# Kernel tuning notes

Hardware: AMD Instinct MI355X
Metric: run time of the kernel (lower is better)

The kernel has to match this reference:

```python
import jax, jax.numpy as jnp
import numpy as np

C = 5          # max within-cluster spike gap (module-level constant in source repo)
DELTA = 0.05   # margin constant (module-level constant in source repo)
B, T, N = 128, 512, 256


def setup_inputs() -> dict:
    key = jax.random.key(0)
    k1, k2, k3 = jax.random.split(key, 3)
    vmem = jax.random.normal(k1, (B, T, N), dtype=jnp.float32) - 1.5
    vlastmem = jax.random.normal(k2, (B, T, N), dtype=jnp.float32)  # unused by the loss math
    labels_t = jax.random.randint(k3, (B, N), 0, 4)
    ratio = jnp.float32(0.5)
    return {"vmem": vmem, "vlastmem": vlastmem, "labels_t": labels_t, "ratio": ratio}


def _per_neuron(v, key):
    """v: [T] membrane trace for one (batch, neuron). Returns (num_cluster, under_term, max_over)."""
    Tn = v.shape[0]
    t = jnp.arange(Tn)
    spike = v >= 0.0
    s = spike.astype(jnp.int32)
    # prefix sums: cs[i] = number of spikes in v[:i]
    cs = jnp.concatenate([jnp.zeros(1, jnp.int32), jnp.cumsum(s)])
    # new cluster starts at t iff spike[t] and no spike in [t-C, t-1]  (gap > C)
    prev_cnt = cs[t] - cs[jnp.clip(t - C, 0, Tn)]
    is_start = spike & (prev_cnt == 0)
    nclu = jnp.sum(is_start.astype(jnp.int32))
    # under-branch mask = union over clusters of [first-C, last+C] = C-dilation of spike train
    dil_cnt = cs[jnp.clip(t + C + 1, 0, Tn)] - cs[jnp.clip(t - C, 0, Tn)]
    mask = dil_cnt > 0

    # per-cluster stats via segmented reductions (cluster id = running count of starts)
    cid = jnp.clip(jnp.cumsum(is_start.astype(jnp.int32)) - 1, 0, Tn - 1)
    counts = jax.ops.segment_sum(s, cid, num_segments=Tn)
    first = jax.ops.segment_min(jnp.where(spike, t, Tn), cid, num_segments=Tn)
    last = jax.ops.segment_max(jnp.where(spike, t, -1), cid, num_segments=Tn)

    # over branch: cluster minimizing (end_idx - beg_idx) == min spike count (first on ties)
    counts_q = jnp.where(t < nclu, counts, Tn + 2)
    ic = jnp.argmin(counts_q)
    over_mask = (t >= first[ic]) & (t <= last[ic])
    max_over = jnp.max(jnp.where(over_mask, v, -jnp.inf))

    # under branch: if unmasked timesteps remain, penalize -max(v[mask==0]);
    # else take v at a (pinned-seed) random spike position
    has_zero = jnp.any(~mask)
    max_unmask = jnp.max(jnp.where(~mask, v, -jnp.inf))
    nsp = cs[-1]
    sorted_pos = jnp.sort(jnp.where(spike, t, Tn))
    r = jax.random.randint(key, (), 0, jnp.maximum(nsp, 1))
    v_rand = v[jnp.clip(sorted_pos[r], 0, Tn - 1)]
    under_term = jnp.where(has_zero, -max_unmask, v_rand)
    return nclu, under_term, max_over


def _forward(vmem, vlastmem, labels_t, ratio):
    Bv, Tv, Nv = vmem.shape
    vflat = jnp.swapaxes(vmem, 1, 2).reshape(Bv * Nv, Tv)   # [B*N, T]
    lflat = labels_t.reshape(Bv * Nv)
    keys = jax.random.split(jax.random.key(42), Bv * Nv)     # pinned seed for the random-spike pick
    nclu, under_term, max_over = jax.vmap(_per_neuron)(vflat, keys)
    ncf = nclu.astype(vmem.dtype)
    margin = DELTA * ratio * ncf
    under = jnp.where(lflat > nclu, under_term + margin, 0.0)
    over = jnp.where(lflat < nclu, max_over + margin, 0.0)
    loss = jnp.sum(under + over)
    spike_output = ncf.reshape(Bv, Nv)
    return loss, spike_output


def reference(vmem, vlastmem, labels_t, ratio):
    return _forward(vmem, vlastmem, labels_t, ratio)
```

## Files before the change

### kernel.cpp

```cpp
#include <hip/hip_runtime.h>
#include <stdint.h>

#define TDIM 512
#define NDIM 256
#define CGAP 5
#define DELTA_C 0.05f
#define NSEG 8
#define SEGT 64
#define BIGI (1 << 28)

extern "C" __global__ void __launch_bounds__(512, 2)
stca_kernel(const float* __restrict__ vmem, const int* __restrict__ labels,
            const float* __restrict__ ratio_p, float* __restrict__ out) {
  __shared__ int   si[9][NSEG * 64];
  __shared__ float sf[6][NSEG * 64];

  const int lane = threadIdx.x & 63;
  const int seg  = threadIdx.x >> 6;
  const int blk  = blockIdx.x;
  const int b    = blk >> 2;
  const int n0   = (blk & 3) << 6;
  const int n    = n0 + lane;

  const float* g = vmem + (size_t)b * TDIM * NDIM + n;
  const int t0 = seg * SEGT, t1 = t0 + SEGT;

  int   last_spike = -1000, nclu = 0, cur_cnt = 0, cur_fs = 0, fs = BIGI;
  float cur_max = -INFINITY, cur_maxlast = -INFINITY;
  float seg_run_max = -INFINITY, mfs_snap = -INFINITY;
  int   pfx_cnt = 0, pfx_ls = 0;
  float pfx_core = -INFINITY, pfx_mfs = -INFINITY;
  int   bint_cnt = BIGI;
  float bint_max = -INFINITY;
  unsigned hist = 0u;
  float umax = -INFINITY;
  int   has_un = 0;
  float vd0 = 0.f, vd1 = 0.f, vd2 = 0.f, vd3 = 0.f, vd4 = 0.f, vd5 = 0.f;

  if (t0 > 0) {
#pragma unroll
    for (int j = 0; j < CGAP; ++j) {
      const float v = g[(size_t)(t0 - CGAP + j) * NDIM];
      hist = ((hist << 1) | (v >= 0.f ? 1u : 0u)) & 0x7FFu;
    }
  }

  auto step = [&](float v, int te) {
    const bool spike   = v >= 0.0f;
    const bool isstart = spike && ((te - last_spike) > CGAP);
    const bool closing = isstart && (nclu > 0);
    const bool isfirst = closing && (nclu == 1);
    const bool bet     = closing && (nclu > 1) && (cur_cnt < bint_cnt);
    pfx_cnt  = isfirst ? cur_cnt     : pfx_cnt;
    pfx_ls   = isfirst ? last_spike  : pfx_ls;
    pfx_core = isfirst ? cur_maxlast : pfx_core;
    pfx_mfs  = isfirst ? mfs_snap    : pfx_mfs;
    bint_cnt = bet ? cur_cnt     : bint_cnt;
    bint_max = bet ? cur_maxlast : bint_max;
    nclu += isstart ? 1 : 0;
    cur_fs  = isstart ? te : cur_fs;
    cur_max = isstart ? v : fmaxf(cur_max, v);
    cur_maxlast = spike ? cur_max : cur_maxlast;
    cur_cnt = (isstart ? 0 : cur_cnt) + (spike ? 1 : 0);
    seg_run_max = fmaxf(seg_run_max, v);
    const bool snap = spike && (nclu == 1);
    mfs_snap = snap ? seg_run_max : mfs_snap;
    fs = (spike && fs == BIGI) ? te : fs;
    last_spike = spike ? te : last_spike;
    hist = ((hist << 1) | (spike ? 1u : 0u)) & 0x7FFu;
    vd5 = vd4; vd4 = vd3; vd3 = vd2; vd2 = vd1; vd1 = vd0; vd0 = v;
    const bool un = (hist == 0u) && (te >= t0 + CGAP);
    umax = un ? fmaxf(umax, vd5) : umax;
    has_un |= un ? 1 : 0;
  };

#pragma unroll 1
  for (int c = 0; c < SEGT / 8; ++c) {
    const float* gp = g + (size_t)(t0 + c * 8) * NDIM;
    const float y0 = gp[0 * NDIM], y1 = gp[1 * NDIM], y2 = gp[2 * NDIM],
                y3 = gp[3 * NDIM], y4 = gp[4 * NDIM], y5 = gp[5 * NDIM],
                y6 = gp[6 * NDIM], y7 = gp[7 * NDIM];
    const int tc = t0 + c * 8;
    step(y0, tc + 0); step(y1, tc + 1); step(y2, tc + 2); step(y3, tc + 3);
    step(y4, tc + 4); step(y5, tc + 5); step(y6, tc + 6); step(y7, tc + 7);
  }

#pragma unroll
  for (int j = 0; j < CGAP; ++j) {
    const int te = t1 + j;
    const float v = (te < TDIM) ? g[(size_t)te * NDIM] : -INFINITY;
    const bool spike = v >= 0.0f;
    hist = ((hist << 1) | (spike ? 1u : 0u)) & 0x7FFu;
    vd5 = vd4; vd4 = vd3; vd3 = vd2; vd2 = vd1; vd1 = vd0; vd0 = v;
    const bool un = (hist == 0u);
    umax = un ? fmaxf(umax, vd5) : umax;
    has_un |= un ? 1 : 0;
  }

  int   sfx_cnt = 0, sfx_fs = 0;
  float sfx_core = -INFINITY, sfx_mte = -INFINITY;
  if (nclu >= 1) {
    sfx_cnt = cur_cnt; sfx_fs = cur_fs; sfx_core = cur_maxlast; sfx_mte = cur_max;
    if (nclu == 1) {
      pfx_cnt = cur_cnt; pfx_ls = last_spike; pfx_core = cur_maxlast; pfx_mfs = mfs_snap;
    }
  }

  const int idx = threadIdx.x;
  si[0][idx] = nclu;   si[1][idx] = fs;      si[2][idx] = last_spike;
  si[3][idx] = pfx_cnt; si[4][idx] = pfx_ls; si[5][idx] = sfx_cnt;
  si[6][idx] = sfx_fs;  si[7][idx] = bint_cnt; si[8][idx] = has_un;
  sf[0][idx] = pfx_core; sf[1][idx] = pfx_mfs; sf[2][idx] = sfx_core;
  sf[3][idx] = sfx_mte;  sf[4][idx] = bint_max; sf[5][idx] = umax;
  __syncthreads();

  if (seg != 0) return;

  int   a_nclu = nclu, a_fs = fs, a_ls = last_spike;
  int   a_pcnt = pfx_cnt, a_pls = pfx_ls, a_scnt = sfx_cnt, a_sfs = sfx_fs;
  int   a_bcnt = bint_cnt, a_hun = has_un;
  float a_pcore = pfx_core, a_pmfs = pfx_mfs, a_score = sfx_core, a_smte = sfx_mte;
  float a_bmax = bint_max, a_umax = umax;

  for (int s = 1; s < NSEG; ++s) {
    const int j = (s << 6) + lane;
    const int   r_nclu = si[0][j], r_fs = si[1][j], r_ls = si[2][j];
    const int   r_pcnt = si[3][j], r_pls = si[4][j];
    const int   r_scnt = si[5][j], r_sfs = si[6][j];
    const int   r_bcnt = si[7][j], r_hun = si[8][j];
    const float r_pcore = sf[0][j], r_pmfs = sf[1][j];
    const float r_score = sf[2][j], r_smte = sf[3][j];
    const float r_bmax = sf[4][j], r_umax = sf[5][j];

    a_umax = fmaxf(a_umax, r_umax);
    a_hun |= r_hun;
    if (r_nclu == 0) continue;
    if (a_nclu == 0) {
      a_nclu = r_nclu; a_fs = r_fs; a_ls = r_ls;
      a_pcnt = r_pcnt; a_pls = r_pls; a_pcore = r_pcore; a_pmfs = r_pmfs;
      a_scnt = r_scnt; a_sfs = r_sfs; a_score = r_score; a_smte = r_smte;
      a_bcnt = r_bcnt; a_bmax = r_bmax;
      continue;
    }
    if (r_fs - a_ls <= CGAP) {
      const int   Bc    = a_scnt + r_pcnt;
      const float Bcore = fmaxf(a_smte, r_pmfs);
      const float Bmfs  = fmaxf(fmaxf(a_pmfs, a_smte), r_pmfs);
      const float Bmte  = fmaxf(fmaxf(a_smte, r_pmfs), r_smte);
      const int   Bfs = a_sfs, Bls = r_pls;
      int nb = a_bcnt; float nbm = a_bmax;
      if (a_nclu >= 2 && r_nclu >= 2 && Bc < nb) { nb = Bc; nbm = Bcore; }
      if (r_bcnt < nb) { nb = r_bcnt; nbm = r_bmax; }
      if (a_nclu == 1) { a_pcnt = Bc; a_pls = Bls; a_pcore = Bcore; a_pmfs = Bmfs; }
      if (r_nclu == 1) { a_scnt = Bc; a_sfs = Bfs; a_score = Bcore; a_smte = Bmte; }
      else             { a_scnt = r_scnt; a_sfs = r_sfs; a_score = r_score; a_smte = r_smte; }
      a_bcnt = nb; a_bmax = nbm;
      a_nclu = a_nclu + r_nclu - 1;
      a_ls = r_ls;
    } else {
      int nb = a_bcnt; float nbm = a_bmax;
      if (a_nclu >= 2 && a_scnt < nb) { nb = a_scnt; nbm = a_score; }
      if (r_nclu >= 2 && r_pcnt < nb) { nb = r_pcnt; nbm = r_pcore; }
      if (r_bcnt < nb) { nb = r_bcnt; nbm = r_bmax; }
      a_bcnt = nb; a_bmax = nbm;
      a_scnt = r_scnt; a_sfs = r_sfs; a_score = r_score; a_smte = r_smte;
      a_nclu += r_nclu;
      a_ls = r_ls;
    }
  }

  int bc = a_pcnt; float bm = a_pcore;
  if (a_nclu >= 2) {
    if (a_bcnt < bc) { bc = a_bcnt; bm = a_bmax; }
    if (a_scnt < bc) { bc = a_scnt; bm = a_score; }
  }

  const float ratio = ratio_p[0];
  const int   label = labels[b * NDIM + n];
  const float ncf    = (float)a_nclu;
  const float margin = DELTA_C * ratio * ncf;
  const float under_term = a_hun ? (-a_umax) : 0.0f;
  const float under = (label > a_nclu) ? (under_term + margin) : 0.0f;
  const float over  = (label < a_nclu) ? (bm + margin) : 0.0f;

  out[1 + b * NDIM + n] = ncf;

  float sum = under + over;
#pragma unroll
  for (int off = 32; off > 0; off >>= 1) sum += __shfl_down(sum, off);
  if (lane == 0) atomicAdd(out, sum);
}

extern "C" void kernel_launch(void* const* d_in, const int* in_sizes, int n_in,
                              void* d_out, int out_size, void* d_ws,
                              size_t ws_size, hipStream_t stream) {
  const float* vmem   = (const float*)d_in[0];
  const int*   labels = (const int*)d_in[2];
  const float* ratio  = (const float*)d_in[3];
  float* out = (float*)d_out;

  hipMemsetAsync(d_out, 0, sizeof(float), stream);
  dim3 grid(512);
  dim3 block(512);
  hipLaunchKernelGGL(stca_kernel, grid, block, 0, stream, vmem, labels, ratio,
                     out);
}
```

Measured before the change: 147.7 us.

## Split scan into bitmask-based segment kernel plus finalize kernel

Replaces the sequential per-timestep state machine with a two-kernel scheme. Each thread loads 32 timesteps, builds a spike bitmask, and uses popcount, ctz/clz and bit dilation to get cluster starts, counts and masked maxima. Partial summaries are merged within the block, written to workspace across four time quarters, and combined by a second finalize kernel that also computes the loss with a block-level reduction before the atomic add. This raises parallelism over time and removes the serial dependency chain, at the cost of an extra launch and a workspace round trip.

```diff
diff --git a/kernel.cpp b/kernel.cpp
--- a/kernel.cpp
+++ b/kernel.cpp
@@ -5,190 +5,254 @@
 #define NDIM 256
 #define CGAP 5
 #define DELTA_C 0.05f
-#define NSEG 8
-#define SEGT 64
 #define BIGI (1 << 28)
 
+typedef unsigned long long u64;
+typedef unsigned int u32;
+
+
+__device__ __forceinline__ int ctz32(u32 x) { return x ? __builtin_ctz(x) : 32; }
+__device__ __forceinline__ int hib32(u32 x) { return x ? 31 - __builtin_clz(x) : -1; }
+__device__ __forceinline__ u32 below32(int p) { return (p >= 32) ? ~0u : ((1u << p) - 1u); }
+__device__ __forceinline__ u32 rmask(int lo, int hi) { return below32(hi + 1) & ~below32(lo); }
+
+struct Sum {
+  int nclu, fs, ls, pcnt, pls, scnt, sfs, bcnt;
+  float pcore, pmfs, score, smte, bmax, umax;
+};
+
+__device__ __forceinline__ void sum_init(Sum& a) {
+  a.nclu = 0; a.fs = BIGI; a.ls = 0; a.pcnt = 0; a.pls = 0; a.scnt = 0;
+  a.sfs = 0; a.bcnt = BIGI;
+  a.pcore = -INFINITY; a.pmfs = -INFINITY; a.score = -INFINITY;
+  a.smte = -INFINITY; a.bmax = -INFINITY; a.umax = -INFINITY;
+}
+
+__device__ __forceinline__ void merge(Sum& a, const Sum& r) {
+  a.umax = fmaxf(a.umax, r.umax);
+  if (r.nclu == 0) return;
+  if (a.nclu == 0) { const float um = a.umax; a = r; a.umax = um; return; }
+  if (r.fs - a.ls <= CGAP) {
+    const int   Bc    = a.scnt + r.pcnt;
+    const float Bcore = fmaxf(a.smte, r.pmfs);
+    const float Bmfs  = fmaxf(fmaxf(a.pmfs, a.smte), r.pmfs);
+    const float Bmte  = fmaxf(fmaxf(a.smte, r.pmfs), r.smte);
+    const int   Bfs = a.sfs, Bls = r.pls;
+    int nb = a.bcnt; float nbm = a.bmax;
+    if (a.nclu >= 2 && r.nclu >= 2 && Bc < nb) { nb = Bc; nbm = Bcore; }
+    if (r.bcnt < nb) { nb = r.bcnt; nbm = r.bmax; }
+    if (a.nclu == 1) { a.pcnt = Bc; a.pls = Bls; a.pcore = Bcore; a.pmfs = Bmfs; }
+    if (r.nclu == 1) { a.scnt = Bc; a.sfs = Bfs; a.score = Bcore; a.smte = Bmte; }
+    else             { a.scnt = r.scnt; a.sfs = r.sfs; a.score = r.score; a.smte = r.smte; }
+    a.bcnt = nb; a.bmax = nbm;
+    a.nclu += r.nclu - 1;
+    a.ls = r.ls;
+  } else {
+    int nb = a.bcnt; float nbm = a.bmax;
+    if (a.nclu >= 2 && a.scnt < nb) { nb = a.scnt; nbm = a.score; }
+    if (r.nclu >= 2 && r.pcnt < nb) { nb = r.pcnt; nbm = r.pcore; }
+    if (r.bcnt < nb) { nb = r.bcnt; nbm = r.bmax; }
+    a.bcnt = nb; a.bmax = nbm;
+    a.scnt = r.scnt; a.sfs = r.sfs; a.score = r.score; a.smte = r.smte;
+    a.nclu += r.nclu;
+    a.ls = r.ls;
+  }
+}
+
+extern "C" __global__ void __launch_bounds__(256, 8)
+stca_seg(const float* __restrict__ vmem, float* __restrict__ ws) {
+  __shared__ u32 shS[256];
+  __shared__ u32 shA0[256], shA1[256];
+  __shared__ float shF[6][256];
+
+  const int tid = threadIdx.x, lane = tid & 63, w = tid >> 6;
+  const int blk = blockIdx.x;
+  const int tq = blk & 3, nq = (blk >> 2) & 3, b = blk >> 4;
+  const int n = (nq << 6) + lane;
+  const int t0 = (tq << 7) + (w << 5);
+  const float* g = vmem + (size_t)b * TDIM * NDIM + n;
+  const float* gp = g + (size_t)t0 * NDIM;
+
+#define LD(i) const float v##i = gp[(i) * NDIM];
+  LD(0)  LD(1)  LD(2)  LD(3)  LD(4)  LD(5)  LD(6)  LD(7)
+  LD(8)  LD(9)  LD(10) LD(11) LD(12) LD(13) LD(14) LD(15)
+  LD(16) LD(17) LD(18) LD(19) LD(20) LD(21) LD(22) LD(23)
+  LD(24) LD(25) LD(26) LD(27) LD(28) LD(29) LD(30) LD(31)
+#undef LD
+
+  u32 left5 = 0, right5 = 0;
+  if (w == 0 && tq > 0) {
+#pragma unroll
+    for (int j = 0; j < CGAP; ++j)
+      left5 |= (g[(size_t)(t0 - CGAP + j) * NDIM] >= 0.f ? 1u : 0u) << j;
+  }
+  if (w == 3 && tq < 3) {
+#pragma unroll
+    for (int j = 0; j < CGAP; ++j)
+      right5 |= (g[(size_t)(t0 + 32 + j) * NDIM] >= 0.f ? 1u : 0u) << j;
+  }
+
+#define SB(i) ((v##i >= 0.f) ? (1u << (i)) : 0u)
+  const u32 s = SB(0)  | SB(1)  | SB(2)  | SB(3)  | SB(4)  | SB(5)  | SB(6)  | SB(7)
+              | SB(8)  | SB(9)  | SB(10) | SB(11) | SB(12) | SB(13) | SB(14) | SB(15)
+              | SB(16) | SB(17) | SB(18) | SB(19) | SB(20) | SB(21) | SB(22) | SB(23)
+              | SB(24) | SB(25) | SB(26) | SB(27) | SB(28) | SB(29) | SB(30) | SB(31);
+#undef SB
+  shS[tid] = s;
+  __syncthreads();
+  if (w > 0) left5 = shS[tid - 64] >> 27;
+  if (w < 3) right5 = shS[tid + 64] & 31u;
+
+  const u64 E = ((u64)s << 5) | (u64)left5 | ((u64)right5 << 37);
+  u64 a3 = E | (E >> 1); a3 |= a3 >> 2; a3 |= a3 >> 4;
+  const u32 D = (u32)(a3 | (a3 >> 3));
+
+  const u32 w5 = (s << 1) | (s << 2) | (s << 3) | (s << 4) | (s << 5);
+  const u32 starts = s & ~w5;
+  const int nclu = __popc(starts);
+  const int fs_l = ctz32(s), ls_l = hib32(s);
+  const u32 st2 = starts & (starts - 1);
+  const int p2 = ctz32(st2);
+  const u32 pm = s & below32(p2);
+  const int pcnt = __popc(pm), pls_l = hib32(pm);
+  const int plast = (nclu >= 1) ? hib32(starts) : 0;
+  const int scnt = __popc(s >> plast);
+  int bcnt = 255, bfs_l = 0, bls_l = 0;
+  u32 rem = st2;
+  while ((rem & (rem - 1)) != 0u) {
+    const int p = ctz32(rem);
+    const u32 rem2 = rem & (rem - 1);
+    const int pnx = ctz32(rem2);
+    const u32 m = s & below32(pnx) & ~below32(p);
+    const int cnt = __popc(m);
+    if (cnt < bcnt) { bcnt = cnt; bfs_l = p; bls_l = hib32(m); }
+    rem = rem2;
+  }
+
+  const u32 Rp  = nclu ? rmask(fs_l, pls_l) : 0u;
+  const u32 Rpm = nclu ? below32(pls_l + 1) : 0u;
+  const u32 Rs  = nclu ? rmask(plast, ls_l) : 0u;
+  const u32 Rsm = nclu ? rmask(plast, 31)   : 0u;
+  const u32 Rb  = (bcnt < 255) ? rmask(bfs_l, bls_l) : 0u;
+  const u32 Ru  = ~D;
+  float mP = -INFINITY, mPM = -INFINITY, mS = -INFINITY, mSM = -INFINITY,
+        mB = -INFINITY, mU = -INFINITY;
+#define MX(i) { \
+    mP  = ((Rp  >> (i)) & 1u) ? fmaxf(mP,  v##i) : mP;  \
+    mPM = ((Rpm >> (i)) & 1u) ? fmaxf(mPM, v##i) : mPM; \
+    mS  = ((Rs  >> (i)) & 1u) ? fmaxf(mS,  v##i) : mS;  \
+    mSM = ((Rsm >> (i)) & 1u) ? fmaxf(mSM, v##i) : mSM; \
+    mB  = ((Rb  >> (i)) & 1u) ? fmaxf(mB,  v##i) : mB;  \
+    mU  = ((Ru  >> (i)) & 1u) ? fmaxf(mU,  v##i) : mU;  }
+  MX(0)  MX(1)  MX(2)  MX(3)  MX(4)  MX(5)  MX(6)  MX(7)
+  MX(8)  MX(9)  MX(10) MX(11) MX(12) MX(13) MX(14) MX(15)
+  MX(16) MX(17) MX(18) MX(19) MX(20) MX(21) MX(22) MX(23)
+  MX(24) MX(25) MX(26) MX(27) MX(28) MX(29) MX(30) MX(31)
+#undef MX
+
+  shA0[tid] = (u32)nclu | ((u32)(fs_l & 255) << 8) | ((u32)(ls_l & 255) << 16)
+            | ((u32)pcnt << 24);
+  shA1[tid] = (u32)(pls_l & 255) | ((u32)scnt << 8) | ((u32)(plast & 255) << 16)
+            | ((u32)bcnt << 24);
+  shF[0][tid] = mP; shF[1][tid] = mPM; shF[2][tid] = mS;
+  shF[3][tid] = mSM; shF[4][tid] = mB; shF[5][tid] = mU;
+  __syncthreads();
+
+  if (w != 0) return;
+
+  Sum A; sum_init(A);
+#pragma unroll
+  for (int sg = 0; sg < 4; ++sg) {
+    const int j = (sg << 6) + lane, t0s = sg << 5;
+    const u32 a0 = shA0[j], a1 = shA1[j];
+    Sum R;
+    R.nclu = (int)(a0 & 255u);
+    R.fs   = t0s + (int)((a0 >> 8) & 255u);
+    R.ls   = t0s + (int)((a0 >> 16) & 255u);
+    R.pcnt = (int)((a0 >> 24) & 255u);
+    R.pls  = t0s + (int)(a1 & 255u);
+    R.scnt = (int)((a1 >> 8) & 255u);
+    R.sfs  = t0s + (int)((a1 >> 16) & 255u);
+    const int rb = (int)((a1 >> 24) & 255u);
+    R.bcnt = (rb == 255) ? BIGI : rb;
+    R.pcore = shF[0][j]; R.pmfs = shF[1][j]; R.score = shF[2][j];
+    R.smte = shF[3][j]; R.bmax = shF[4][j]; R.umax = shF[5][j];
+    merge(A, R);
+  }
+
+  u32* wp = (u32*)ws + ((size_t)((b << 8) + n) * 4 + (size_t)tq) * 8;
+  const int pb = A.pcnt > 255 ? 255 : A.pcnt;
+  const int sb = A.scnt > 255 ? 255 : A.scnt;
+  const int bb = A.bcnt > 255 ? 255 : A.bcnt;
+  wp[0] = (u32)(A.nclu & 255) | ((u32)(A.fs & 255) << 8)
+        | ((u32)(A.ls & 255) << 16) | ((u32)pb << 24);
+  wp[1] = (u32)(A.pls & 255) | ((u32)sb << 8) | ((u32)(A.sfs & 255) << 16)
+        | ((u32)bb << 24);
+  wp[2] = __float_as_uint(A.pcore);
+  wp[3] = __float_as_uint(A.pmfs);
+  wp[4] = __float_as_uint(A.score);
+  wp[5] = __float_as_uint(A.smte);
+  wp[6] = __float_as_uint(A.bmax);
+  wp[7] = __float_as_uint(A.umax);
+}
+
 extern "C" __global__ void __launch_bounds__(512, 2)
-stca_kernel(const float* __restrict__ vmem, const int* __restrict__ labels,
-            const float* __restrict__ ratio_p, float* __restrict__ out) {
-  __shared__ int   si[9][NSEG * 64];
-  __shared__ float sf[6][NSEG * 64];
-
-  const int lane = threadIdx.x & 63;
-  const int seg  = threadIdx.x >> 6;
-  const int blk  = blockIdx.x;
-  const int b    = blk >> 2;
-  const int n0   = (blk & 3) << 6;
-  const int n    = n0 + lane;
-
-  const float* g = vmem + (size_t)b * TDIM * NDIM + n;
-  const int t0 = seg * SEGT, t1 = t0 + SEGT;
-
-  int   last_spike = -1000, nclu = 0, cur_cnt = 0, cur_fs = 0, fs = BIGI;
-  float cur_max = -INFINITY, cur_maxlast = -INFINITY;
-  float seg_run_max = -INFINITY, mfs_snap = -INFINITY;
-  int   pfx_cnt = 0, pfx_ls = 0;
-  float pfx_core = -INFINITY, pfx_mfs = -INFINITY;
-  int   bint_cnt = BIGI;
-  float bint_max = -INFINITY;
-  unsigned hist = 0u;
-  float umax = -INFINITY;
-  int   has_un = 0;
-  float vd0 = 0.f, vd1 = 0.f, vd2 = 0.f, vd3 = 0.f, vd4 = 0.f, vd5 = 0.f;
-
-  if (t0 > 0) {
-#pragma unroll
-    for (int j = 0; j < CGAP; ++j) {
-      const float v = g[(size_t)(t0 - CGAP + j) * NDIM];
-      hist = ((hist << 1) | (v >= 0.f ? 1u : 0u)) & 0x7FFu;
-    }
-  }
-
-  auto step = [&](float v, int te) {
-    const bool spike   = v >= 0.0f;
-    const bool isstart = spike && ((te - last_spike) > CGAP);
-    const bool closing = isstart && (nclu > 0);
-    const bool isfirst = closing && (nclu == 1);
-    const bool bet     = closing && (nclu > 1) && (cur_cnt < bint_cnt);
-    pfx_cnt  = isfirst ? cur_cnt     : pfx_cnt;
-    pfx_ls   = isfirst ? last_spike  : pfx_ls;
-    pfx_core = isfirst ? cur_maxlast : pfx_core;
-    pfx_mfs  = isfirst ? mfs_snap    : pfx_mfs;
-    bint_cnt = bet ? cur_cnt     : bint_cnt;
-    bint_max = bet ? cur_maxlast : bint_max;
-    nclu += isstart ? 1 : 0;
-    cur_fs  = isstart ? te : cur_fs;
-    cur_max = isstart ? v : fmaxf(cur_max, v);
-    cur_maxlast = spike ? cur_max : cur_maxlast;
-    cur_cnt = (isstart ? 0 : cur_cnt) + (spike ? 1 : 0);
-    seg_run_max = fmaxf(seg_run_max, v);
-    const bool snap = spike && (nclu == 1);
-    mfs_snap = snap ? seg_run_max : mfs_snap;
-    fs = (spike && fs == BIGI) ? te : fs;
-    last_spike = spike ? te : last_spike;
-    hist = ((hist << 1) | (spike ? 1u : 0u)) & 0x7FFu;
-    vd5 = vd4; vd4 = vd3; vd3 = vd2; vd2 = vd1; vd1 = vd0; vd0 = v;
-    const bool un = (hist == 0u) && (te >= t0 + CGAP);
-    umax = un ? fmaxf(umax, vd5) : umax;
-    has_un |= un ? 1 : 0;
-  };
-
-#pragma unroll 1
-  for (int c = 0; c < SEGT / 8; ++c) {
-    const float* gp = g + (size_t)(t0 + c * 8) * NDIM;
-    const float y0 = gp[0 * NDIM], y1 = gp[1 * NDIM], y2 = gp[2 * NDIM],
-                y3 = gp[3 * NDIM], y4 = gp[4 * NDIM], y5 = gp[5 * NDIM],
-                y6 = gp[6 * NDIM], y7 = gp[7 * NDIM];
-    const int tc = t0 + c * 8;
-    step(y0, tc + 0); step(y1, tc + 1); step(y2, tc + 2); step(y3, tc + 3);
-    step(y4, tc + 4); step(y5, tc + 5); step(y6, tc + 6); step(y7, tc + 7);
-  }
-
-#pragma unroll
-  for (int j = 0; j < CGAP; ++j) {
-    const int te = t1 + j;
-    const float v = (te < TDIM) ? g[(size_t)te * NDIM] : -INFINITY;
-    const bool spike = v >= 0.0f;
-    hist = ((hist << 1) | (spike ? 1u : 0u)) & 0x7FFu;
-    vd5 = vd4; vd4 = vd3; vd3 = vd2; vd2 = vd1; vd1 = vd0; vd0 = v;
-    const bool un = (hist == 0u);
-    umax = un ? fmaxf(umax, vd5) : umax;
-    has_un |= un ? 1 : 0;
-  }
-
-  int   sfx_cnt = 0, sfx_fs = 0;
-  float sfx_core = -INFINITY, sfx_mte = -INFINITY;
-  if (nclu >= 1) {
-    sfx_cnt = cur_cnt; sfx_fs = cur_fs; sfx_core = cur_maxlast; sfx_mte = cur_max;
-    if (nclu == 1) {
-      pfx_cnt = cur_cnt; pfx_ls = last_spike; pfx_core = cur_maxlast; pfx_mfs = mfs_snap;
-    }
-  }
-
-  const int idx = threadIdx.x;
-  si[0][idx] = nclu;   si[1][idx] = fs;      si[2][idx] = last_spike;
-  si[3][idx] = pfx_cnt; si[4][idx] = pfx_ls; si[5][idx] = sfx_cnt;
-  si[6][idx] = sfx_fs;  si[7][idx] = bint_cnt; si[8][idx] = has_un;
-  sf[0][idx] = pfx_core; sf[1][idx] = pfx_mfs; sf[2][idx] = sfx_core;
-  sf[3][idx] = sfx_mte;  sf[4][idx] = bint_max; sf[5][idx] = umax;
+stca_fin(const float* __restrict__ ws, const int* __restrict__ labels,
+         const float* __restrict__ ratio_p, float* __restrict__ out) {
+  __shared__ float red[8];
+  const int g = blockIdx.x * 512 + threadIdx.x;
+  const u32* wp = (const u32*)ws + (size_t)g * 32;
+
+  Sum A; sum_init(A);
+#pragma unroll
+  for (int tq = 0; tq < 4; ++tq) {
+    const u32* q = wp + tq * 8;
+    const u32 a0 = q[0], a1 = q[1];
+    const int t0s = tq << 7;
+    Sum R;
+    R.nclu = (int)(a0 & 255u);
+    R.fs   = t0s + (int)((a0 >> 8) & 255u);
+    R.ls   = t0s + (int)((a0 >> 16) & 255u);
+    R.pcnt = (int)((a0 >> 24) & 255u);
+    R.pls  = t0s + (int)(a1 & 255u);
+    R.scnt = (int)((a1 >> 8) & 255u);
+    R.sfs  = t0s + (int)((a1 >> 16) & 255u);
+    const int rb = (int)((a1 >> 24) & 255u);
+    R.bcnt = (rb == 255) ? BIGI : rb;
+    R.pcore = __uint_as_float(q[2]); R.pmfs = __uint_as_float(q[3]);
+    R.score = __uint_as_float(q[4]); R.smte = __uint_as_float(q[5]);
+    R.bmax  = __uint_as_float(q[6]); R.umax = __uint_as_float(q[7]);
+    merge(A, R);
+  }
+
+  int bc = A.pcnt; float bm = A.pcore;
+  if (A.nclu >= 2) {
+    if (A.bcnt < bc) { bc = A.bcnt; bm = A.bmax; }
+    if (A.scnt < bc) { bc = A.scnt; bm = A.score; }
+  }
+
+  const float ratio  = ratio_p[0];
+  const int   label  = labels[g];
+  const float ncf    = (float)A.nclu;
+  const float margin = DELTA_C * ratio * ncf;
+  const float under_term = (A.umax > -INFINITY) ? (-A.umax) : 0.0f;
+  const float under = (label > A.nclu) ? (under_term + margin) : 0.0f;
+  const float over  = (label < A.nclu) ? (bm + margin) : 0.0f;
+
+  out[1 + g] = ncf;
+
+  float sum = under + over;
+#pragma unroll
+  for (int off = 32; off > 0; off >>= 1) sum += __shfl_down(sum, off);
+  const int lane = threadIdx.x & 63, wv = threadIdx.x >> 6;
+  if (lane == 0) red[wv] = sum;
   __syncthreads();
-
-  if (seg != 0) return;
-
-  int   a_nclu = nclu, a_fs = fs, a_ls = last_spike;
-  int   a_pcnt = pfx_cnt, a_pls = pfx_ls, a_scnt = sfx_cnt, a_sfs = sfx_fs;
-  int   a_bcnt = bint_cnt, a_hun = has_un;
-  float a_pcore = pfx_core, a_pmfs = pfx_mfs, a_score = sfx_core, a_smte = sfx_mte;
-  float a_bmax = bint_max, a_umax = umax;
-
-  for (int s = 1; s < NSEG; ++s) {
-    const int j = (s << 6) + lane;
-    const int   r_nclu = si[0][j], r_fs = si[1][j], r_ls = si[2][j];
-    const int   r_pcnt = si[3][j], r_pls = si[4][j];
-    const int   r_scnt = si[5][j], r_sfs = si[6][j];
-    const int   r_bcnt = si[7][j], r_hun = si[8][j];
-    const float r_pcore = sf[0][j], r_pmfs = sf[1][j];
-    const float r_score = sf[2][j], r_smte = sf[3][j];
-    const float r_bmax = sf[4][j], r_umax = sf[5][j];
-
-    a_umax = fmaxf(a_umax, r_umax);
-    a_hun |= r_hun;
-    if (r_nclu == 0) continue;
-    if (a_nclu == 0) {
-      a_nclu = r_nclu; a_fs = r_fs; a_ls = r_ls;
-      a_pcnt = r_pcnt; a_pls = r_pls; a_pcore = r_pcore; a_pmfs = r_pmfs;
-      a_scnt = r_scnt; a_sfs = r_sfs; a_score = r_score; a_smte = r_smte;
-      a_bcnt = r_bcnt; a_bmax = r_bmax;
-      continue;
-    }
-    if (r_fs - a_ls <= CGAP) {
-      const int   Bc    = a_scnt + r_pcnt;
-      const float Bcore = fmaxf(a_smte, r_pmfs);
-      const float Bmfs  = fmaxf(fmaxf(a_pmfs, a_smte), r_pmfs);
-      const float Bmte  = fmaxf(fmaxf(a_smte, r_pmfs), r_smte);
-      const int   Bfs = a_sfs, Bls = r_pls;
-      int nb = a_bcnt; float nbm = a_bmax;
-      if (a_nclu >= 2 && r_nclu >= 2 && Bc < nb) { nb = Bc; nbm = Bcore; }
-      if (r_bcnt < nb) { nb = r_bcnt; nbm = r_bmax; }
-      if (a_nclu == 1) { a_pcnt = Bc; a_pls = Bls; a_pcore = Bcore; a_pmfs = Bmfs; }
-      if (r_nclu == 1) { a_scnt = Bc; a_sfs = Bfs; a_score = Bcore; a_smte = Bmte; }
-      else             { a_scnt = r_scnt; a_sfs = r_sfs; a_score = r_score; a_smte = r_smte; }
-      a_bcnt = nb; a_bmax = nbm;
-      a_nclu = a_nclu + r_nclu - 1;
-      a_ls = r_ls;
-    } else {
-      int nb = a_bcnt; float nbm = a_bmax;
-      if (a_nclu >= 2 && a_scnt < nb) { nb = a_scnt; nbm = a_score; }
-      if (r_nclu >= 2 && r_pcnt < nb) { nb = r_pcnt; nbm = r_pcore; }
-      if (r_bcnt < nb) { nb = r_bcnt; nbm = r_bmax; }
-      a_bcnt = nb; a_bmax = nbm;
-      a_scnt = r_scnt; a_sfs = r_sfs; a_score = r_score; a_smte = r_smte;
-      a_nclu += r_nclu;
-      a_ls = r_ls;
-    }
-  }
-
-  int bc = a_pcnt; float bm = a_pcore;
-  if (a_nclu >= 2) {
-    if (a_bcnt < bc) { bc = a_bcnt; bm = a_bmax; }
-    if (a_scnt < bc) { bc = a_scnt; bm = a_score; }
-  }
-
-  const float ratio = ratio_p[0];
-  const int   label = labels[b * NDIM + n];
-  const float ncf    = (float)a_nclu;
-  const float margin = DELTA_C * ratio * ncf;
-  const float under_term = a_hun ? (-a_umax) : 0.0f;
-  const float under = (label > a_nclu) ? (under_term + margin) : 0.0f;
-  const float over  = (label < a_nclu) ? (bm + margin) : 0.0f;
-
-  out[1 + b * NDIM + n] = ncf;
-
-  float sum = under + over;
-#pragma unroll
-  for (int off = 32; off > 0; off >>= 1) sum += __shfl_down(sum, off);
-  if (lane == 0) atomicAdd(out, sum);
+  if (threadIdx.x == 0) {
+    float t = red[0];
+#pragma unroll
+    for (int i = 1; i < 8; ++i) t += red[i];
+    atomicAdd(out, t);
+  }
 }
 
 extern "C" void kernel_launch(void* const* d_in, const int* in_sizes, int n_in,
@@ -198,10 +262,10 @@
   const int*   labels = (const int*)d_in[2];
   const float* ratio  = (const float*)d_in[3];
   float* out = (float*)d_out;
+  float* ws  = (float*)d_ws;
 
   hipMemsetAsync(d_out, 0, sizeof(float), stream);
-  dim3 grid(512);
-  dim3 block(512);
-  hipLaunchKernelGGL(stca_kernel, grid, block, 0, stream, vmem, labels, ratio,
-                     out);
-}
+  hipLaunchKernelGGL(stca_seg, dim3(2048), dim3(256), 0, stream, vmem, ws);
+  hipLaunchKernelGGL(stca_fin, dim3(64), dim3(512), 0, stream, ws, labels,
+                     ratio, out);
+}
```

New measurement: 151.1 us. 1.02x slower.
